# Performance work log

Hardware: AMD Instinct MI355X
Metric: run time of the kernel (lower is better)

Reference implementation:

```python
import jax, jax.numpy as jnp
import numpy as np

B, D_IN, EXPERT_DIM, N_EXPERT, N_TASK = 16384, 1024, 256, 8, 4


def setup_inputs() -> dict:
    key = jax.random.key(0)
    k1, k2, k3 = jax.random.split(key, 3)
    x = jax.random.normal(k1, (B, D_IN), dtype=jnp.float32)
    # Glorot-ish scaling for weights
    We = jax.random.normal(k2, (N_EXPERT, D_IN, EXPERT_DIM), dtype=jnp.float32) * (1.0 / np.sqrt(D_IN))
    be = jnp.zeros((N_EXPERT, EXPERT_DIM), dtype=jnp.float32)
    Wg = jax.random.normal(k3, (N_TASK, D_IN, N_EXPERT), dtype=jnp.float32) * (1.0 / np.sqrt(D_IN))
    bg = jnp.zeros((N_TASK, N_EXPERT), dtype=jnp.float32)
    return {"x": x, "We": We, "be": be, "Wg": Wg, "bg": bg}


def reference(x, We, be, Wg, bg):
    # Experts: grouped GEMM -> [B, n_expert, expert_dim]
    E = jax.nn.relu(jnp.einsum("bd,edh->beh", x, We) + be[None, :, :])
    # Gates: [B, n_task, n_expert], softmax over experts
    G = jax.nn.softmax(jnp.einsum("bd,tde->bte", x, Wg) + bg[None, :, :], axis=-1)
    # Gated combine per task: towers[t] = E^T @ g_t -> [n_task, B, expert_dim]
    towers = jnp.einsum("beh,bte->tbh", E, G)
    return towers  # stacked version of the original list of [B, expert_dim] towers
```

## Files before the change

kernel.cpp:

```cpp
#include <hip/hip_runtime.h>

#define B_ROWS 16384
#define D_IN   1024
#define H_DIM  256
#define N_EXP  8
#define N_TASK 4
#define NKT    16

typedef short bf16x8 __attribute__((ext_vector_type(8)));
typedef float f32x4  __attribute__((ext_vector_type(4)));
typedef unsigned short u16x8 __attribute__((ext_vector_type(8)));

static __device__ __forceinline__ unsigned short f2bf(float f) {
  unsigned int u = __float_as_uint(f);
  u += 0x7fffu + ((u >> 16) & 1u);
  return (unsigned short)(u >> 16);
}
static __device__ __forceinline__ float bf2f(unsigned short u) {
  return __uint_as_float(((unsigned int)u) << 16);
}

#define WS_XB   0u
#define WS_WET  33554432u
#define WS_WGT  37748736u
#define WS_G    37814272u
#define WS_E    39911424u

__global__ void k_prep_w(const float* __restrict__ We, const float* __restrict__ Wg,
                         unsigned short* __restrict__ We_t, unsigned short* __restrict__ Wg_t) {
  int bid = blockIdx.x;
  int t = threadIdx.x;
  if (bid < 512) {
    int e = bid >> 6;
    int tl = bid & 63;
    int k0 = (tl >> 2) * 64, h0 = (tl & 3) * 64;
    __shared__ unsigned short tile[64][72];
    const float* src = We + (size_t)e * (D_IN * H_DIM);
#pragma unroll
    for (int i = 0; i < 4; ++i) {
      int kk = (t >> 4) + i * 16;
      int hh = (t & 15) * 4;
      float4 v = *(const float4*)(src + (size_t)(k0 + kk) * H_DIM + h0 + hh);
      tile[hh + 0][kk] = f2bf(v.x);
      tile[hh + 1][kk] = f2bf(v.y);
      tile[hh + 2][kk] = f2bf(v.z);
      tile[hh + 3][kk] = f2bf(v.w);
    }
    __syncthreads();
    unsigned short* dst = We_t + (size_t)e * (H_DIM * D_IN);
#pragma unroll
    for (int i = 0; i < 4; ++i) {
      int hh = (t >> 4) + i * 16;
      int kk = (t & 15) * 4;
      ushort4 u = *(const ushort4*)&tile[hh][kk];
      *(ushort4*)(dst + (size_t)(h0 + hh) * D_IN + k0 + kk) = u;
    }
  } else {
    int n = bid - 512;
    int tsk = n >> 3, e = n & 7;
    int k = t * 4;
    const float* src = Wg + (size_t)tsk * (D_IN * 8) + e;
    ushort4 u;
    u.x = f2bf(src[(size_t)(k + 0) * 8]);
    u.y = f2bf(src[(size_t)(k + 1) * 8]);
    u.z = f2bf(src[(size_t)(k + 2) * 8]);
    u.w = f2bf(src[(size_t)(k + 3) * 8]);
    *(ushort4*)(Wg_t + (size_t)n * D_IN + k) = u;
  }
}

__global__ void k_gates(const float* __restrict__ x,
                        const unsigned short* __restrict__ Wg_t,
                        unsigned short* __restrict__ x_b,
                        const float* __restrict__ bg,
                        float* __restrict__ G) {
  __shared__ unsigned short xs[64][136];
  __shared__ unsigned short wgs[32][136];
  int m0 = blockIdx.x * 64;
  int t = threadIdx.x;
  int wv = t >> 6, l = t & 63;
  f32x4 acc0 = {0.f, 0.f, 0.f, 0.f}, acc1 = {0.f, 0.f, 0.f, 0.f};

  for (int k0 = 0; k0 < D_IN; k0 += 128) {
    {
      int r = t >> 2;
      int cb = (t & 3) * 32;
      const float* p = x + (size_t)(m0 + r) * D_IN + k0 + cb;
      unsigned short* q = x_b + (size_t)(m0 + r) * D_IN + k0 + cb;
#pragma unroll
      for (int i = 0; i < 8; ++i) {
        float4 v = *(const float4*)(p + i * 4);
        ushort4 u;
        u.x = f2bf(v.x); u.y = f2bf(v.y); u.z = f2bf(v.z); u.w = f2bf(v.w);
        *(ushort4*)&xs[r][cb + i * 4] = u;
        *(ushort4*)(q + i * 4) = u;
      }
    }
    {
      int n = t >> 3;
      int kk = (t & 7) * 16;
      const unsigned short* p = Wg_t + (size_t)n * D_IN + k0 + kk;
#pragma unroll
      for (int i = 0; i < 4; ++i)
        *(ushort4*)&wgs[n][kk + i * 4] = *(const ushort4*)(p + i * 4);
    }
    __syncthreads();
#pragma unroll
    for (int kk = 0; kk < 4; ++kk) {
      bf16x8 a  = *(const bf16x8*)&xs[wv * 16 + (l & 15)][kk * 32 + (l >> 4) * 8];
      bf16x8 b0 = *(const bf16x8*)&wgs[(l & 15)][kk * 32 + (l >> 4) * 8];
      bf16x8 b1 = *(const bf16x8*)&wgs[16 + (l & 15)][kk * 32 + (l >> 4) * 8];
      acc0 = __builtin_amdgcn_mfma_f32_16x16x32_bf16(a, b0, acc0, 0, 0, 0);
      acc1 = __builtin_amdgcn_mfma_f32_16x16x32_bf16(a, b1, acc1, 0, 0, 0);
    }
    __syncthreads();
  }

  int colb = l & 15;
  int rbase = m0 + wv * 16 + (l >> 4) * 4;
  float bga = bg[colb], bgb = bg[16 + colb];
#pragma unroll
  for (int j = 0; j < 4; ++j) {
    float va = acc0[j] + bga;
    float vb = acc1[j] + bgb;
    float mxa = va, mxb = vb;
#pragma unroll
    for (int d = 1; d < 8; d <<= 1) {
      mxa = fmaxf(mxa, __shfl_xor(mxa, d));
      mxb = fmaxf(mxb, __shfl_xor(mxb, d));
    }
    va = __expf(va - mxa); vb = __expf(vb - mxb);
    float sa = va, sb = vb;
#pragma unroll
    for (int d = 1; d < 8; d <<= 1) {
      sa += __shfl_xor(sa, d);
      sb += __shfl_xor(sb, d);
    }
    va /= sa; vb /= sb;
    G[(size_t)(rbase + j) * 32 + colb]      = va;
    G[(size_t)(rbase + j) * 32 + 16 + colb] = vb;
  }
}

__global__ __launch_bounds__(512, 2) void k_expert(const unsigned short* __restrict__ x_b,
                                                   const unsigned short* __restrict__ We_t,
                                                   const float* __restrict__ be,
                                                   unsigned short* __restrict__ E) {
  __shared__ unsigned short As[2][256 * 64];
  __shared__ unsigned short Bs[2][256 * 64];
  int bid = blockIdx.x;
  int t = threadIdx.x;

  int xcd = bid & 7;
  int idx = bid >> 3;
  int m   = xcd * 8 + (idx >> 3);
  int e   = idx & 7;
  int m0  = m * 256;

  int w  = t >> 6, l = t & 63;
  int wm = w >> 2, wn = w & 3;
  int lr = l & 15, lq = l >> 4;

  const unsigned short* Ab = x_b + (size_t)m0 * D_IN;
  const unsigned short* Bb = We_t + (size_t)e * (H_DIM * D_IN);

  const int sr = t >> 3, sg = t & 7;
  const int swz0 = ((lq ^ (lr & 7)) << 3);
  const int swz1 = (((4 + lq) ^ (lr & 7)) << 3);
  const int arow0 = (wm * 128 + lr) << 6;
  const int brow0 = (wn * 64 + lr) << 6;

  f32x4 acc[8][4];
#pragma unroll
  for (int i = 0; i < 8; ++i)
#pragma unroll
    for (int j = 0; j < 4; ++j) acc[i][j] = (f32x4){0.f, 0.f, 0.f, 0.f};

#define STAGE_A(cb, kt, h)                                                                       \
  do {                                                                                           \
    int r0_ = (h) * 128 + sr;                                                                    \
    int r1_ = r0_ + 64;                                                                          \
    __builtin_amdgcn_global_load_lds(                                                            \
        (const __attribute__((address_space(1))) void*)(Ab + (size_t)r0_ * D_IN + (kt) * 64 +    \
                                                        ((sg ^ (r0_ & 7)) << 3)),                \
        (__attribute__((address_space(3))) void*)(&As[(cb)][r0_ * 64 + sg * 8]), 16, 0, 0);      \
    __builtin_amdgcn_global_load_lds(                                                            \
        (const __attribute__((address_space(1))) void*)(Ab + (size_t)r1_ * D_IN + (kt) * 64 +    \
                                                        ((sg ^ (r1_ & 7)) << 3)),                \
        (__attribute__((address_space(3))) void*)(&As[(cb)][r1_ * 64 + sg * 8]), 16, 0, 0);      \
  } while (0)
#define STAGE_B(cb, kt, h)                                                                       \
  do {                                                                                           \
    int r0_ = (h) * 128 + sr;                                                                    \
    int r1_ = r0_ + 64;                                                                          \
    __builtin_amdgcn_global_load_lds(                                                            \
        (const __attribute__((address_space(1))) void*)(Bb + (size_t)r0_ * D_IN + (kt) * 64 +    \
                                                        ((sg ^ (r0_ & 7)) << 3)),                \
        (__attribute__((address_space(3))) void*)(&Bs[(cb)][r0_ * 64 + sg * 8]), 16, 0, 0);      \
    __builtin_amdgcn_global_load_lds(                                                            \
        (const __attribute__((address_space(1))) void*)(Bb + (size_t)r1_ * D_IN + (kt) * 64 +    \
                                                        ((sg ^ (r1_ & 7)) << 3)),                \
        (__attribute__((address_space(3))) void*)(&Bs[(cb)][r1_ * 64 + sg * 8]), 16, 0, 0);      \
  } while (0)

  STAGE_A(0, 0, 0); STAGE_A(0, 0, 1);
  STAGE_B(0, 0, 0); STAGE_B(0, 0, 1);
  STAGE_B(1, 1, 0); STAGE_B(1, 1, 1);
  asm volatile("s_waitcnt vmcnt(4)" ::: "memory");
  __builtin_amdgcn_s_barrier();

#pragma unroll 2
  for (int kt = 0; kt < NKT; ++kt) {
    int c = kt & 1;
    const unsigned short* Ap = &As[c][0];
    const unsigned short* Bp = &Bs[c][0];
    bf16x8 b0[4], b1[4];
#pragma unroll
    for (int q = 0; q < 4; ++q) {
      if (q == 0) {
#pragma unroll
        for (int fn = 0; fn < 4; ++fn) {
          b0[fn] = *(const bf16x8*)(Bp + brow0 + fn * 1024 + swz0);
          b1[fn] = *(const bf16x8*)(Bp + brow0 + fn * 1024 + swz1);
        }
      }
      bf16x8 a00 = *(const bf16x8*)(Ap + arow0 + (2 * q) * 1024 + swz0);
      bf16x8 a01 = *(const bf16x8*)(Ap + arow0 + (2 * q) * 1024 + swz1);
      bf16x8 a10 = *(const bf16x8*)(Ap + arow0 + (2 * q + 1) * 1024 + swz0);
      bf16x8 a11 = *(const bf16x8*)(Ap + arow0 + (2 * q + 1) * 1024 + swz1);
      if (q == 0)      { if (kt + 1 < NKT) STAGE_A(c ^ 1, kt + 1, 0); }
      else if (q == 1) { if (kt + 1 < NKT) STAGE_A(c ^ 1, kt + 1, 1); }
      else if (q == 2) { if (kt + 2 < NKT) STAGE_B(c, kt + 2, 0); }
      else             { if (kt + 2 < NKT) STAGE_B(c, kt + 2, 1); }
      __builtin_amdgcn_s_barrier();
      asm volatile("s_waitcnt lgkmcnt(0)" ::: "memory");
      __builtin_amdgcn_s_setprio(1);
#pragma unroll
      for (int fn = 0; fn < 4; ++fn) {
        acc[2 * q][fn]     = __builtin_amdgcn_mfma_f32_16x16x32_bf16(a00, b0[fn], acc[2 * q][fn], 0, 0, 0);
        acc[2 * q][fn]     = __builtin_amdgcn_mfma_f32_16x16x32_bf16(a01, b1[fn], acc[2 * q][fn], 0, 0, 0);
        acc[2 * q + 1][fn] = __builtin_amdgcn_mfma_f32_16x16x32_bf16(a10, b0[fn], acc[2 * q + 1][fn], 0, 0, 0);
        acc[2 * q + 1][fn] = __builtin_amdgcn_mfma_f32_16x16x32_bf16(a11, b1[fn], acc[2 * q + 1][fn], 0, 0, 0);
      }
      __builtin_amdgcn_s_setprio(0);
      if (q == 3) {
        if (kt < NKT - 2)        asm volatile("s_waitcnt vmcnt(4)" ::: "memory");
        else if (kt == NKT - 2)  asm volatile("s_waitcnt vmcnt(0)" ::: "memory");
      }
      __builtin_amdgcn_s_barrier();
    }
  }
#undef STAGE_A
#undef STAGE_B

  float bev[4];
#pragma unroll
  for (int fn = 0; fn < 4; ++fn)
    bev[fn] = be[e * H_DIM + wn * 64 + fn * 16 + lr];
#pragma unroll
  for (int fm = 0; fm < 8; ++fm) {
#pragma unroll
    for (int fn = 0; fn < 4; ++fn) {
      int col = wn * 64 + fn * 16 + lr;
#pragma unroll
      for (int j = 0; j < 4; ++j) {
        int row = m0 + wm * 128 + fm * 16 + lq * 4 + j;
        float vv = fmaxf(acc[fm][fn][j] + bev[fn], 0.f);
        E[(size_t)row * (N_EXP * H_DIM) + e * H_DIM + col] = f2bf(vv);
      }
    }
  }
}

__global__ void k_combine(const unsigned short* __restrict__ E, const float* __restrict__ G,
                          float* __restrict__ out) {
  int t = threadIdx.x;
  int wv = t >> 6, l = t & 63;
  int r = blockIdx.x * 8 + wv * 2 + (l >> 5);
  int h0 = (l & 31) * 8;
  const unsigned short* er = E + (size_t)r * (N_EXP * H_DIM) + h0;
  const float* g = G + (size_t)r * 32;
  float garr[32];
#pragma unroll
  for (int c = 0; c < 8; ++c) {
    float4 a = *(const float4*)(g + c * 4);
    garr[c * 4 + 0] = a.x; garr[c * 4 + 1] = a.y;
    garr[c * 4 + 2] = a.z; garr[c * 4 + 3] = a.w;
  }
  float acc[4][8];
#pragma unroll
  for (int tk = 0; tk < 4; ++tk)
#pragma unroll
    for (int i = 0; i < 8; ++i) acc[tk][i] = 0.f;
#pragma unroll
  for (int e = 0; e < 8; ++e) {
    u16x8 u = *(const u16x8*)(er + e * H_DIM);
#pragma unroll
    for (int i = 0; i < 8; ++i) {
      float f = bf2f((unsigned short)u[i]);
#pragma unroll
      for (int tk = 0; tk < 4; ++tk)
        acc[tk][i] += garr[tk * 8 + e] * f;
    }
  }
#pragma unroll
  for (int tk = 0; tk < 4; ++tk) {
    float* o = out + ((size_t)tk * B_ROWS + r) * H_DIM + h0;
    *(float4*)(o)     = make_float4(acc[tk][0], acc[tk][1], acc[tk][2], acc[tk][3]);
    *(float4*)(o + 4) = make_float4(acc[tk][4], acc[tk][5], acc[tk][6], acc[tk][7]);
  }
}

extern "C" void kernel_launch(void* const* d_in, const int* in_sizes, int n_in,
                              void* d_out, int out_size, void* d_ws, size_t ws_size,
                              hipStream_t stream) {
  const float* x  = (const float*)d_in[0];
  const float* We = (const float*)d_in[1];
  const float* be = (const float*)d_in[2];
  const float* Wg = (const float*)d_in[3];
  const float* bg = (const float*)d_in[4];
  float* out = (float*)d_out;
  char* ws = (char*)d_ws;
  unsigned short* x_b  = (unsigned short*)(ws + WS_XB);
  unsigned short* We_t = (unsigned short*)(ws + WS_WET);
  unsigned short* Wg_t = (unsigned short*)(ws + WS_WGT);
  float*          G    = (float*)(ws + WS_G);
  unsigned short* E    = (unsigned short*)(ws + WS_E);

  k_prep_w<<<544, 256, 0, stream>>>(We, Wg, We_t, Wg_t);
  k_gates<<<B_ROWS / 64, 256, 0, stream>>>(x, Wg_t, x_b, bg, G);
  k_expert<<<512, 512, 0, stream>>>(x_b, We_t, be, E);
  k_combine<<<B_ROWS / 8, 256, 0, stream>>>(E, G, out);
}
```

Before: 227.8 us.

## Fuse gated combine into expert GEMM epilogue and drop E intermediate

After: 208.1 us. -8.6%, faster.

```diff
diff --git a/kernel.cpp b/kernel.cpp
--- a/kernel.cpp
+++ b/kernel.cpp
@@ -16,17 +16,15 @@
   u += 0x7fffu + ((u >> 16) & 1u);
   return (unsigned short)(u >> 16);
 }
-static __device__ __forceinline__ float bf2f(unsigned short u) {
-  return __uint_as_float(((unsigned int)u) << 16);
-}
 
 #define WS_XB   0u
 #define WS_WET  33554432u
 #define WS_WGT  37748736u
-#define WS_G    37814272u
-#define WS_E    39911424u
-
-__global__ void k_prep_w(const float* __restrict__ We, const float* __restrict__ Wg,
+#define WS_GT   37814272u
+
+__global__ void k_prep_w(const float* __restrict__ x, const float* __restrict__ We,
+                         const float* __restrict__ Wg,
+                         unsigned short* __restrict__ x_b,
                          unsigned short* __restrict__ We_t, unsigned short* __restrict__ Wg_t) {
   int bid = blockIdx.x;
   int t = threadIdx.x;
@@ -55,7 +53,7 @@
       ushort4 u = *(const ushort4*)&tile[hh][kk];
       *(ushort4*)(dst + (size_t)(h0 + hh) * D_IN + k0 + kk) = u;
     }
-  } else {
+  } else if (bid < 544) {
     int n = bid - 512;
     int tsk = n >> 3, e = n & 7;
     int k = t * 4;
@@ -66,14 +64,23 @@
     u.z = f2bf(src[(size_t)(k + 2) * 8]);
     u.w = f2bf(src[(size_t)(k + 3) * 8]);
     *(ushort4*)(Wg_t + (size_t)n * D_IN + k) = u;
-  }
-}
-
-__global__ void k_gates(const float* __restrict__ x,
+  } else {
+    size_t base = (size_t)(bid - 544) * 2048 + (size_t)t * 8;
+    float4 v0 = *(const float4*)(x + base);
+    float4 v1 = *(const float4*)(x + base + 4);
+    u16x8 u;
+    u[0] = (short)f2bf(v0.x); u[1] = (short)f2bf(v0.y);
+    u[2] = (short)f2bf(v0.z); u[3] = (short)f2bf(v0.w);
+    u[4] = (short)f2bf(v1.x); u[5] = (short)f2bf(v1.y);
+    u[6] = (short)f2bf(v1.z); u[7] = (short)f2bf(v1.w);
+    *(u16x8*)(x_b + base) = u;
+  }
+}
+
+__global__ void k_gates(const unsigned short* __restrict__ x_b,
                         const unsigned short* __restrict__ Wg_t,
-                        unsigned short* __restrict__ x_b,
                         const float* __restrict__ bg,
-                        float* __restrict__ G) {
+                        float* __restrict__ Gt) {
   __shared__ unsigned short xs[64][136];
   __shared__ unsigned short wgs[32][136];
   int m0 = blockIdx.x * 64;
@@ -85,16 +92,10 @@
     {
       int r = t >> 2;
       int cb = (t & 3) * 32;
-      const float* p = x + (size_t)(m0 + r) * D_IN + k0 + cb;
-      unsigned short* q = x_b + (size_t)(m0 + r) * D_IN + k0 + cb;
-#pragma unroll
-      for (int i = 0; i < 8; ++i) {
-        float4 v = *(const float4*)(p + i * 4);
-        ushort4 u;
-        u.x = f2bf(v.x); u.y = f2bf(v.y); u.z = f2bf(v.z); u.w = f2bf(v.w);
-        *(ushort4*)&xs[r][cb + i * 4] = u;
-        *(ushort4*)(q + i * 4) = u;
-      }
+      const unsigned short* p = x_b + (size_t)(m0 + r) * D_IN + k0 + cb;
+#pragma unroll
+      for (int i = 0; i < 4; ++i)
+        *(u16x8*)&xs[r][cb + i * 8] = *(const u16x8*)(p + i * 8);
     }
     {
       int n = t >> 3;
@@ -137,15 +138,16 @@
       sb += __shfl_xor(sb, d);
     }
     va /= sa; vb /= sb;
-    G[(size_t)(rbase + j) * 32 + colb]      = va;
-    G[(size_t)(rbase + j) * 32 + 16 + colb] = vb;
+    Gt[(size_t)colb * B_ROWS + rbase + j]        = va;
+    Gt[(size_t)(16 + colb) * B_ROWS + rbase + j] = vb;
   }
 }
 
 __global__ __launch_bounds__(512, 2) void k_expert(const unsigned short* __restrict__ x_b,
                                                    const unsigned short* __restrict__ We_t,
                                                    const float* __restrict__ be,
-                                                   unsigned short* __restrict__ E) {
+                                                   const float* __restrict__ Gt,
+                                                   float* __restrict__ out) {
   __shared__ unsigned short As[2][256 * 64];
   __shared__ unsigned short Bs[2][256 * 64];
   int bid = blockIdx.x;
@@ -154,7 +156,7 @@
   int xcd = bid & 7;
   int idx = bid >> 3;
   int m   = xcd * 8 + (idx >> 3);
-  int e   = idx & 7;
+  int hs  = idx & 7;
   int m0  = m * 256;
 
   int w  = t >> 6, l = t & 63;
@@ -162,13 +164,21 @@
   int lr = l & 15, lq = l >> 4;
 
   const unsigned short* Ab = x_b + (size_t)m0 * D_IN;
-  const unsigned short* Bb = We_t + (size_t)e * (H_DIM * D_IN);
 
   const int sr = t >> 3, sg = t & 7;
   const int swz0 = ((lq ^ (lr & 7)) << 3);
   const int swz1 = (((4 + lq) ^ (lr & 7)) << 3);
   const int arow0 = (wm * 128 + lr) << 6;
   const int brow0 = (wn * 64 + lr) << 6;
+
+  size_t bsrc[4];
+#pragma unroll
+  for (int q2 = 0; q2 < 4; ++q2) {
+    int rq = q2 * 64 + sr;
+    int me = (rq >> 3) & 7;
+    int mh = hs * 32 + ((rq >> 6) & 3) * 8 + (rq & 7);
+    bsrc[q2] = (size_t)(me * H_DIM + mh) * D_IN + (size_t)((sg ^ (rq & 7)) << 3);
+  }
 
   f32x4 acc[8][4];
 #pragma unroll
@@ -194,12 +204,10 @@
     int r0_ = (h) * 128 + sr;                                                                    \
     int r1_ = r0_ + 64;                                                                          \
     __builtin_amdgcn_global_load_lds(                                                            \
-        (const __attribute__((address_space(1))) void*)(Bb + (size_t)r0_ * D_IN + (kt) * 64 +    \
-                                                        ((sg ^ (r0_ & 7)) << 3)),                \
+        (const __attribute__((address_space(1))) void*)(We_t + bsrc[2 * (h)] + (kt) * 64),       \
         (__attribute__((address_space(3))) void*)(&Bs[(cb)][r0_ * 64 + sg * 8]), 16, 0, 0);      \
     __builtin_amdgcn_global_load_lds(                                                            \
-        (const __attribute__((address_space(1))) void*)(Bb + (size_t)r1_ * D_IN + (kt) * 64 +    \
-                                                        ((sg ^ (r1_ & 7)) << 3)),                \
+        (const __attribute__((address_space(1))) void*)(We_t + bsrc[2 * (h) + 1] + (kt) * 64),   \
         (__attribute__((address_space(3))) void*)(&Bs[(cb)][r1_ * 64 + sg * 8]), 16, 0, 0);      \
   } while (0)
 
@@ -253,61 +261,43 @@
 #undef STAGE_A
 #undef STAGE_B
 
+  int hi = lr >> 3, h7 = lr & 7;
+  int hglob = hs * 32 + wn * 8 + h7;
   float bev[4];
 #pragma unroll
   for (int fn = 0; fn < 4; ++fn)
-    bev[fn] = be[e * H_DIM + wn * 64 + fn * 16 + lr];
+    bev[fn] = be[(2 * fn + hi) * H_DIM + hglob];
 #pragma unroll
   for (int fm = 0; fm < 8; ++fm) {
-#pragma unroll
-    for (int fn = 0; fn < 4; ++fn) {
-      int col = wn * 64 + fn * 16 + lr;
-#pragma unroll
-      for (int j = 0; j < 4; ++j) {
-        int row = m0 + wm * 128 + fm * 16 + lq * 4 + j;
-        float vv = fmaxf(acc[fm][fn][j] + bev[fn], 0.f);
-        E[(size_t)row * (N_EXP * H_DIM) + e * H_DIM + col] = f2bf(vv);
+    int r0 = m0 + wm * 128 + fm * 16 + lq * 4;
+    float vv[4][4];
+#pragma unroll
+    for (int fn = 0; fn < 4; ++fn)
+#pragma unroll
+      for (int j = 0; j < 4; ++j)
+        vv[fn][j] = fmaxf(acc[fm][fn][j] + bev[fn], 0.f);
+#pragma unroll
+    for (int tk = 0; tk < 4; ++tk) {
+      float4 gv[4];
+#pragma unroll
+      for (int fn = 0; fn < 4; ++fn)
+        gv[fn] = *(const float4*)(Gt + (size_t)(tk * 8 + 2 * fn + hi) * B_ROWS + r0);
+      float s0 = gv[0].x * vv[0][0] + gv[1].x * vv[1][0] + gv[2].x * vv[2][0] + gv[3].x * vv[3][0];
+      float s1 = gv[0].y * vv[0][1] + gv[1].y * vv[1][1] + gv[2].y * vv[2][1] + gv[3].y * vv[3][1];
+      float s2 = gv[0].z * vv[0][2] + gv[1].z * vv[1][2] + gv[2].z * vv[2][2] + gv[3].z * vv[3][2];
+      float s3 = gv[0].w * vv[0][3] + gv[1].w * vv[1][3] + gv[2].w * vv[2][3] + gv[3].w * vv[3][3];
+      s0 += __shfl_xor(s0, 8);
+      s1 += __shfl_xor(s1, 8);
+      s2 += __shfl_xor(s2, 8);
+      s3 += __shfl_xor(s3, 8);
+      if ((tk >> 1) == hi) {
+        float* o = out + ((size_t)tk * B_ROWS + r0) * H_DIM + hglob;
+        o[0]                 = s0;
+        o[(size_t)H_DIM]     = s1;
+        o[(size_t)H_DIM * 2] = s2;
+        o[(size_t)H_DIM * 3] = s3;
       }
     }
-  }
-}
-
-__global__ void k_combine(const unsigned short* __restrict__ E, const float* __restrict__ G,
-                          float* __restrict__ out) {
-  int t = threadIdx.x;
-  int wv = t >> 6, l = t & 63;
-  int r = blockIdx.x * 8 + wv * 2 + (l >> 5);
-  int h0 = (l & 31) * 8;
-  const unsigned short* er = E + (size_t)r * (N_EXP * H_DIM) + h0;
-  const float* g = G + (size_t)r * 32;
-  float garr[32];
-#pragma unroll
-  for (int c = 0; c < 8; ++c) {
-    float4 a = *(const float4*)(g + c * 4);
-    garr[c * 4 + 0] = a.x; garr[c * 4 + 1] = a.y;
-    garr[c * 4 + 2] = a.z; garr[c * 4 + 3] = a.w;
-  }
-  float acc[4][8];
-#pragma unroll
-  for (int tk = 0; tk < 4; ++tk)
-#pragma unroll
-    for (int i = 0; i < 8; ++i) acc[tk][i] = 0.f;
-#pragma unroll
-  for (int e = 0; e < 8; ++e) {
-    u16x8 u = *(const u16x8*)(er + e * H_DIM);
-#pragma unroll
-    for (int i = 0; i < 8; ++i) {
-      float f = bf2f((unsigned short)u[i]);
-#pragma unroll
-      for (int tk = 0; tk < 4; ++tk)
-        acc[tk][i] += garr[tk * 8 + e] * f;
-    }
-  }
-#pragma unroll
-  for (int tk = 0; tk < 4; ++tk) {
-    float* o = out + ((size_t)tk * B_ROWS + r) * H_DIM + h0;
-    *(float4*)(o)     = make_float4(acc[tk][0], acc[tk][1], acc[tk][2], acc[tk][3]);
-    *(float4*)(o + 4) = make_float4(acc[tk][4], acc[tk][5], acc[tk][6], acc[tk][7]);
   }
 }
 
@@ -324,11 +314,9 @@
   unsigned short* x_b  = (unsigned short*)(ws + WS_XB);
   unsigned short* We_t = (unsigned short*)(ws + WS_WET);
   unsigned short* Wg_t = (unsigned short*)(ws + WS_WGT);
-  float*          G    = (float*)(ws + WS_G);
-  unsigned short* E    = (unsigned short*)(ws + WS_E);
-
-  k_prep_w<<<544, 256, 0, stream>>>(We, Wg, We_t, Wg_t);
-  k_gates<<<B_ROWS / 64, 256, 0, stream>>>(x, Wg_t, x_b, bg, G);
-  k_expert<<<512, 512, 0, stream>>>(x_b, We_t, be, E);
-  k_combine<<<B_ROWS / 8, 256, 0, stream>>>(E, G, out);
-}
+  float*          Gt   = (float*)(ws + WS_GT);
+
+  k_prep_w<<<544 + 8192, 256, 0, stream>>>(x, We, Wg, x_b, We_t, Wg_t);
+  k_gates<<<B_ROWS / 64, 256, 0, stream>>>(x_b, Wg_t, bg, Gt);
+  k_expert<<<512, 512, 0, stream>>>(x_b, We_t, be, Gt, out);
+}
```
